# Kernel optimization log

Measured on AMD Instinct MI355X. Metric: run time of the kernel, lower is better.

The kernel has to match this reference:

```python
import jax, jax.numpy as jnp
import numpy as np

HID = 256
BATCH = 16384
L_K = 4


def _mixture(lst, Ws):
    # lst: [B, 4, H] candidate tensors; Ws: [H] scoring vector (Linear(H,1,bias=False))
    scores = jnp.einsum('bkh,h->bk', lst, Ws)            # [B, 4]
    w = jax.nn.softmax(scores, axis=-1)                  # softmax over the l=4 candidates
    out = jnp.einsum('bk,bkh->bh', w, lst)               # [B, H] mixture
    s = scores.sum(axis=0)                               # [4] summed over batch
    idx = jnp.argmax(s).astype(jnp.int32)                # routing decision
    ss = jnp.sort(s)
    margin = ss[-1] - ss[-2]                             # top-2 margin
    return out, idx, margin


def setup_inputs() -> dict:
    key = jax.random.key(0)
    ks = jax.random.split(key, 6)
    bound = 1.0 / np.sqrt(HID)
    x = jax.random.normal(ks[0], (BATCH, 1, HID), dtype=jnp.float32)
    h = jax.random.normal(ks[1], (BATCH, 1, HID), dtype=jnp.float32)
    L = jax.random.uniform(ks[2], (L_K, HID, HID), dtype=jnp.float32, minval=-bound, maxval=bound)
    R = jax.random.uniform(ks[3], (L_K, HID, HID), dtype=jnp.float32, minval=-bound, maxval=bound)
    # k=3 slots are initialized to identity / zero bias in the torch module
    L = L.at[3].set(jnp.eye(HID, dtype=jnp.float32))
    R = R.at[3].set(jnp.eye(HID, dtype=jnp.float32))
    b = jnp.zeros((L_K, HID), dtype=jnp.float32)
    Ws = jax.random.normal(ks[4], (HID,), dtype=jnp.float32) * bound
    return {'x': x, 'h': h, 'L': L, 'R': R, 'b': b, 'Ws': Ws}


def reference(x, h, L, R, b, Ws):
    x2 = x[:, 0, :]  # [B, H]
    h2 = h[:, 0, :]  # [B, H]

    z1 = jax.nn.sigmoid(x2 @ L[0] + h2 @ R[0] + b[0])
    r = jax.nn.sigmoid(x2 @ L[1] + h2 @ R[1] + b[1])
    z2 = jax.nn.sigmoid(x2 @ L[0] + h2 @ R[0] + b[0])  # identical expression in the source

    def lin(A, Bv):
        # candidate set: A @ L[k] + Bv @ R[k] + b[k] for k in 0..3 -> [B, 4, H]
        return jnp.einsum('bh,khd->bkd', A, L) + jnp.einsum('bh,khd->bkd', Bv, R) + b[None]

    rh, i1, m1 = _mixture(lin(h2, r), Ws)
    h_tilde, i2, m2 = _mixture(lin(x2, rh), Ws)

    omz_cand = 1.0 - (jnp.einsum('bh,khd->bkd', z1, R) + b[None])
    oneMinusZ1, i3, m3 = _mixture(omz_cand, Ws)

    zh_cand = jnp.einsum('bh,khd->bkd', h_tilde, L) * jnp.einsum('bh,khd->bkd', oneMinusZ1, R) + b[None]
    zh_tilde, i4, m4 = _mixture(zh_cand, Ws)

    z2h_cand = jnp.einsum('bh,khd->bkd', h2, L) * jnp.einsum('bh,khd->bkd', z2, R) + b[None]
    z2h, i5, m5 = _mixture(z2h_cand, Ws)

    h_next, i6, m6 = _mixture(lin(zh_tilde, z2h), Ws)

    G_structure = jnp.concatenate([
        jnp.array([0, 1, 0], dtype=jnp.int32),
        jnp.stack([i1, i2, i3, i4, i5, i6]),
    ])
    G_node = jnp.stack([z1, r, z2, rh, h_tilde, oneMinusZ1, zh_tilde, z2h, h_next], axis=1)  # [B, 9, H]
    margins = jnp.stack([m1, m2, m3, m4, m5, m6])
    return h_next[:, None, :], G_structure, G_node, margins
```

## Files before the change

### kernel.cpp

```cpp
#include <hip/hip_runtime.h>

typedef __bf16 bf16_t;
typedef bf16_t bf16x8 __attribute__((ext_vector_type(8)));
typedef float f32x4 __attribute__((ext_vector_type(4)));

#define BATCH 16384
#define HID 256

__device__ __forceinline__ ushort f2b(float f) {
  union { float f; unsigned u; } v; v.f = f;
  unsigned u = v.u;
  unsigned r = (u + 0x7fffu + ((u >> 16) & 1u)) >> 16;
  return (ushort)r;
}
__device__ __forceinline__ float b2f(ushort u) {
  union { unsigned u; float f; } v; v.u = ((unsigned)u) << 16; return v.f;
}
__device__ __forceinline__ void loadbf4(const ushort* __restrict__ p, float* o) {
  uint2 q = *(const uint2*)p;
  o[0] = b2f((ushort)(q.x & 0xffffu));
  o[1] = b2f((ushort)(q.x >> 16));
  o[2] = b2f((ushort)(q.y & 0xffffu));
  o[3] = b2f((ushort)(q.y >> 16));
}
__device__ __forceinline__ uint2 packbf4(const float* v) {
  uint2 q;
  q.x = (unsigned)f2b(v[0]) | ((unsigned)f2b(v[1]) << 16);
  q.y = (unsigned)f2b(v[2]) | ((unsigned)f2b(v[3]) << 16);
  return q;
}

__global__ __launch_bounds__(256)
void f2b2_kernel(const float* __restrict__ a, const float* __restrict__ b,
                 ushort* __restrict__ oa, ushort* __restrict__ ob) {
  int bid = blockIdx.x;
  const float* in = (bid < 4096) ? a : b;
  ushort* out     = (bid < 4096) ? oa : ob;
  int t = (bid & 4095) * 256 + threadIdx.x;
  float4 v = *(const float4*)(in + (size_t)t * 4);
  float q[4] = {v.x, v.y, v.z, v.w};
  *(uint2*)(out + (size_t)t * 4) = packbf4(q);
}

__global__ __launch_bounds__(256)
void wt2_kernel(const float* __restrict__ L, const float* __restrict__ R,
                ushort* __restrict__ Lt, ushort* __restrict__ Rt) {
  int bid = blockIdx.x;
  const float* W = (bid < 1024) ? L : R;
  ushort* Wt     = (bid < 1024) ? Lt : Rt;
  int idx = (bid & 1023) * 256 + threadIdx.x;
  int c = idx >> 8, hh = idx & 255;
  int ks = c >> 8, d = c & 255;
  Wt[idx] = f2b(W[ks * 65536 + hh * 256 + d]);
}

struct GJob {
  const ushort* A; const ushort* B; ushort* out;
  int nx;
  int nblocks;
};

__global__ __launch_bounds__(256, 4)
void gemm3_kernel(GJob j0, GJob j1, GJob j2, int o1, int o2) {
  __shared__ __align__(16) ushort SH[16384];

  const int bid = blockIdx.x;
  GJob j; int lbid;
  if (bid < o1)      { j = j0; lbid = bid; }
  else if (bid < o2) { j = j1; lbid = bid - o1; }
  else               { j = j2; lbid = bid - o2; }

  const int tid  = threadIdx.x;
  const int lane = tid & 63;
  const int wave = tid >> 6;

  const int qq  = j.nblocks >> 3;
  const int id2 = (lbid & 7) * qq + (lbid >> 3);
  int cn, cm;
  if (j.nx == 8) { cn = id2 & 7; cm = id2 >> 3; }
  else           { cn = id2 & 3; cm = id2 >> 2; }
  const int bm = cm * 128;
  const int bn = cn * 128;

  const int wm   = (wave >> 1) * 64;
  const int wn   = (wave & 1) * 64;
  const int row  = lane & 15;
  const int quad = lane >> 4;
  const int gq   = (quad ^ ((row >> 1) & 3)) << 3;

  const int l4   = lane >> 2;
  const int gsrc = (lane & 3) ^ ((lane >> 3) & 3);

  f32x4 acc[4][4] = {};

  auto stage = [&](int buf, int kt) {
    const int k0 = kt * 32;
    for (int i = 0; i < 2; ++i) {
      const int ci = wave * 2 + i;
      const int r  = ci * 16 + l4;
      __builtin_amdgcn_global_load_lds(
          (const __attribute__((address_space(1))) void*)(j.A + (size_t)(bm + r) * 256 + k0 + gsrc * 8),
          (__attribute__((address_space(3))) void*)&SH[buf * 4096 + ci * 512], 16, 0, 0);
      __builtin_amdgcn_global_load_lds(
          (const __attribute__((address_space(1))) void*)(j.B + (size_t)(bn + r) * 256 + k0 + gsrc * 8),
          (__attribute__((address_space(3))) void*)&SH[8192 + buf * 4096 + ci * 512], 16, 0, 0);
    }
  };

  auto compute = [&](int buf) {
    bf16x8 af[4], bf[4];
    for (int f = 0; f < 4; ++f) {
      const int ar = wm + f * 16 + row;
      af[f] = *(const bf16x8*)&SH[buf * 4096 + ar * 32 + gq];
      const int br = wn + f * 16 + row;
      bf[f] = *(const bf16x8*)&SH[8192 + buf * 4096 + br * 32 + gq];
    }
    __builtin_amdgcn_s_setprio(1);
    for (int ti = 0; ti < 4; ++ti)
      for (int tj = 0; tj < 4; ++tj)
        acc[ti][tj] = __builtin_amdgcn_mfma_f32_16x16x32_bf16(af[ti], bf[tj], acc[ti][tj], 0, 0, 0);
    __builtin_amdgcn_s_setprio(0);
  };

  stage(0, 0);
  __syncthreads();
#pragma unroll
  for (int t = 0; t < 8; ++t) {
    if (t < 7) stage((t + 1) & 1, t + 1);
    __builtin_amdgcn_sched_barrier(0);
    compute(t & 1);
    if (t < 7) __syncthreads();
  }

  __syncthreads();
  const int N = j.nx * 128;
  ushort* cw = &SH[wave * 4096];
  for (int ti = 0; ti < 4; ++ti)
    for (int tj = 0; tj < 4; ++tj)
      for (int r2 = 0; r2 < 4; ++r2) {
        const int r = ti * 16 + quad * 4 + r2;
        const int c = tj * 16 + row;
        cw[r * 64 + ((((c >> 3) ^ (r & 7)) << 3) | (c & 7))] = f2b(acc[ti][tj][r2]);
      }
  for (int it = 0; it < 8; ++it) {
    const int lr = it * 8 + (lane >> 3);
    const int ch = lane & 7;
    const int gp = ch ^ (lr & 7);
    uint4 v = *(const uint4*)&cw[lr * 64 + gp * 8];
    *(uint4*)(j.out + (size_t)(bm + wm + lr) * N + bn + wn + ch * 8) = v;
  }
}

__global__ __launch_bounds__(256)
void sig_kernel(const ushort* __restrict__ P0, const ushort* __restrict__ P2,
                const float* __restrict__ bias, float* __restrict__ gnode,
                ushort* __restrict__ z1b, ushort* __restrict__ rb) {
  int t = blockIdx.x * 256 + threadIdx.x;
  int b = t >> 6;
  int d0 = (t & 63) * 4;
  float xl[4], hr[4], z[4], r[4];
  loadbf4(P0 + (size_t)b * 1024 + d0, xl);
  loadbf4(P2 + (size_t)b * 512 + d0, hr);
  float4 bb = *(const float4*)(bias + d0);
  float bbb[4] = {bb.x, bb.y, bb.z, bb.w};
  for (int i = 0; i < 4; ++i) z[i] = 1.0f / (1.0f + expf(-(xl[i] + hr[i] + bbb[i])));
  size_t g = (size_t)b * 2304 + d0;
  float4 zv = {z[0], z[1], z[2], z[3]};
  *(float4*)(gnode + g) = zv;
  *(float4*)(gnode + g + 512) = zv;
  *(uint2*)(z1b + (size_t)b * 256 + d0) = packbf4(z);
  loadbf4(P0 + (size_t)b * 1024 + 256 + d0, xl);
  loadbf4(P2 + (size_t)b * 512 + 256 + d0, hr);
  float4 b1 = *(const float4*)(bias + 256 + d0);
  float b1b[4] = {b1.x, b1.y, b1.z, b1.w};
  for (int i = 0; i < 4; ++i) r[i] = 1.0f / (1.0f + expf(-(xl[i] + hr[i] + b1b[i])));
  float4 rv = {r[0], r[1], r[2], r[3]};
  *(float4*)(gnode + g + 256) = rv;
  *(uint2*)(rb + (size_t)b * 256 + d0) = packbf4(r);
}

struct MixJob {
  const ushort* P1; const ushort* P2;
  float* gnode; ushort* act; float* hnext; float* part;
  int mode;
};

__global__ __launch_bounds__(256)
void mixN_kernel(MixJob j0, MixJob j1, MixJob j2, const float* __restrict__ bias,
                 const float* __restrict__ Ws) {
  const int jb = blockIdx.x >> 12;
  const MixJob j = (jb == 0) ? j0 : (jb == 1) ? j1 : j2;
  const int lb = blockIdx.x & 4095;

  const int tid  = threadIdx.x;
  const int wave = tid >> 6;
  const int lane = tid & 63;
  const int row  = lb * 4 + wave;
  const int d0   = lane * 4;
  float c[4][4];
  float sp[4];
  float4 w4 = *(const float4*)(Ws + d0);
  float ws4[4] = {w4.x, w4.y, w4.z, w4.w};
  for (int k = 0; k < 4; ++k) {
    float p1[4];
    loadbf4(j.P1 + (size_t)row * 1024 + k * 256 + d0, p1);
    float4 bb = *(const float4*)(bias + k * 256 + d0);
    float bv[4] = {bb.x, bb.y, bb.z, bb.w};
    float v[4];
    if (j.mode == 0) {
      float p2[4];
      loadbf4(j.P2 + (size_t)row * 1024 + k * 256 + d0, p2);
      for (int i = 0; i < 4; ++i) v[i] = p1[i] + p2[i] + bv[i];
    } else if (j.mode == 1) {
      for (int i = 0; i < 4; ++i) v[i] = 1.0f - (p1[i] + bv[i]);
    } else {
      float p2[4];
      loadbf4(j.P2 + (size_t)row * 1024 + k * 256 + d0, p2);
      for (int i = 0; i < 4; ++i) v[i] = p1[i] * p2[i] + bv[i];
    }
    float s = 0.f;
    for (int i = 0; i < 4; ++i) { c[k][i] = v[i]; s += v[i] * ws4[i]; }
    sp[k] = s;
  }
  for (int m = 1; m < 64; m <<= 1)
    for (int k = 0; k < 4; ++k) sp[k] += __shfl_xor(sp[k], m, 64);
  float mx = fmaxf(fmaxf(sp[0], sp[1]), fmaxf(sp[2], sp[3]));
  float e0 = expf(sp[0] - mx), e1 = expf(sp[1] - mx), e2 = expf(sp[2] - mx), e3 = expf(sp[3] - mx);
  float inv = 1.0f / (e0 + e1 + e2 + e3);
  float w0 = e0 * inv, w1 = e1 * inv, w2 = e2 * inv, w3 = e3 * inv;
  float o[4];
  for (int i = 0; i < 4; ++i) o[i] = w0 * c[0][i] + w1 * c[1][i] + w2 * c[2][i] + w3 * c[3][i];
  size_t g = (size_t)row * 2304 + d0;
  float4 ov = {o[0], o[1], o[2], o[3]};
  *(float4*)(j.gnode + g) = ov;
  if (j.act) *(uint2*)(j.act + (size_t)row * 256 + d0) = packbf4(o);
  if (j.hnext) *(float4*)(j.hnext + (size_t)row * 256 + d0) = ov;
  __shared__ float sred[4][4];
  if (lane == 0) for (int k = 0; k < 4; ++k) sred[wave][k] = sp[k];
  __syncthreads();
  if (tid < 4)
    j.part[lb * 4 + tid] = sred[0][tid] + sred[1][tid] + sred[2][tid] + sred[3][tid];
}

__global__ __launch_bounds__(256)
void fin_kernel(const float* __restrict__ part, float* __restrict__ gs,
                float* __restrict__ margins) {
  __shared__ float red[256][4];
  __shared__ float sfin[6][4];
  int tid = threadIdx.x;
  for (int si = 0; si < 6; ++si) {
    float a[4] = {0.f, 0.f, 0.f, 0.f};
    for (int i = 0; i < 16; ++i) {
      const float* p = part + ((size_t)si * 4096 + tid + 256 * i) * 4;
      for (int k = 0; k < 4; ++k) a[k] += p[k];
    }
    for (int k = 0; k < 4; ++k) red[tid][k] = a[k];
    __syncthreads();
    for (int st = 128; st >= 1; st >>= 1) {
      if (tid < st) for (int k = 0; k < 4; ++k) red[tid][k] += red[tid + st][k];
      __syncthreads();
    }
    if (tid == 0) for (int k = 0; k < 4; ++k) sfin[si][k] = red[0][k];
    __syncthreads();
  }
  if (tid == 0) {
    gs[0] = 0.f; gs[1] = 1.f; gs[2] = 0.f;
    for (int si = 0; si < 6; ++si) {
      float s[4] = {sfin[si][0], sfin[si][1], sfin[si][2], sfin[si][3]};
      int idx = 0; float best = s[0];
      for (int k = 1; k < 4; ++k) if (s[k] > best) { best = s[k]; idx = k; }
      float second = -3.4e38f;
      for (int k = 0; k < 4; ++k) if (k != idx) second = fmaxf(second, s[k]);
      gs[3 + si] = (float)idx;
      margins[si] = best - second;
    }
  }
}

extern "C" void kernel_launch(void* const* d_in, const int* in_sizes, int n_in,
                              void* d_out, int out_size, void* d_ws, size_t ws_size,
                              hipStream_t stream) {
  const float* x    = (const float*)d_in[0];
  const float* h    = (const float*)d_in[1];
  const float* L    = (const float*)d_in[2];
  const float* R    = (const float*)d_in[3];
  const float* bias = (const float*)d_in[4];
  const float* Ws   = (const float*)d_in[5];

  float* out        = (float*)d_out;
  float* out_hnext  = out;
  float* out_gs     = out + 4194304;
  float* out_gnode  = out + 4194313;
  float* out_marg   = out + 41943049;

  ushort* P0   = (ushort*)d_ws;
  ushort* P1   = P0 + (size_t)BATCH * 1024;
  ushort* P2   = P1 + (size_t)BATCH * 1024;
  ushort* P3   = P2 + (size_t)BATCH * 1024;
  ushort* x2b  = P3 + (size_t)BATCH * 1024;
  ushort* h2b  = x2b + (size_t)BATCH * HID;
  ushort* z1b  = h2b + (size_t)BATCH * HID;
  ushort* rb   = z1b + (size_t)BATCH * HID;
  ushort* rhb  = rb  + (size_t)BATCH * HID;
  ushort* htb  = rhb + (size_t)BATCH * HID;
  ushort* omzb = htb + (size_t)BATCH * HID;
  ushort* ztb  = omzb + (size_t)BATCH * HID;
  ushort* z2hb = ztb + (size_t)BATCH * HID;
  ushort* Lt   = z2hb + (size_t)BATCH * HID;
  ushort* Rt   = Lt + 1024 * 256;
  float*  part = (float*)(Rt + 1024 * 256);

  f2b2_kernel<<<8192, 256, 0, stream>>>(x, h, x2b, h2b);
  wt2_kernel<<<2048, 256, 0, stream>>>(L, R, Lt, Rt);

  GJob jz = {};

  {
    GJob a = {x2b, Lt, P0, 8, 1024};
    GJob b = {h2b, Lt, P1, 8, 1024};
    GJob c = {h2b, Rt, P2, 4, 512};
    gemm3_kernel<<<2560, 256, 0, stream>>>(a, b, c, 1024, 2048);
  }
  sig_kernel<<<4096, 256, 0, stream>>>(P0, P2, bias, out_gnode, z1b, rb);
  {
    GJob a = {rb,  Rt, P2, 8, 1024};
    GJob b = {z1b, Rt, P3, 8, 1024};
    gemm3_kernel<<<2048, 256, 0, stream>>>(a, b, jz, 1024, 2048);
  }
  {
    MixJob m0 = {P1, P2, out_gnode + 3 * 256, rhb,  nullptr, part + 0 * 16384, 0};
    MixJob m1 = {P3, P3, out_gnode + 5 * 256, omzb, nullptr, part + 2 * 16384, 1};
    MixJob m2 = {P1, P3, out_gnode + 7 * 256, z2hb, nullptr, part + 4 * 16384, 2};
    mixN_kernel<<<12288, 256, 0, stream>>>(m0, m1, m2, bias, Ws);
  }
  {
    GJob a = {rhb,  Rt, P2, 8, 1024};
    GJob b = {omzb, Rt, P3, 8, 1024};
    GJob c = {z2hb, Rt, P1, 8, 1024};
    gemm3_kernel<<<3072, 256, 0, stream>>>(a, b, c, 1024, 2048);
  }
  {
    MixJob m0 = {P0, P2, out_gnode + 4 * 256, htb, nullptr, part + 1 * 16384, 0};
    mixN_kernel<<<4096, 256, 0, stream>>>(m0, m0, m0, bias, Ws);
  }
  {
    GJob a = {htb, Lt, P0, 8, 1024};
    gemm3_kernel<<<1024, 256, 0, stream>>>(a, jz, jz, 1024, 1024);
  }
  {
    MixJob m0 = {P0, P3, out_gnode + 6 * 256, ztb, nullptr, part + 3 * 16384, 2};
    mixN_kernel<<<4096, 256, 0, stream>>>(m0, m0, m0, bias, Ws);
  }
  {
    GJob a = {ztb, Lt, P2, 8, 1024};
    gemm3_kernel<<<1024, 256, 0, stream>>>(a, jz, jz, 1024, 1024);
  }
  {
    MixJob m0 = {P2, P1, out_gnode + 8 * 256, nullptr, out_hnext, part + 5 * 16384, 0};
    mixN_kernel<<<4096, 256, 0, stream>>>(m0, m0, m0, bias, Ws);
  }
  fin_kernel<<<1, 256, 0, stream>>>(part, out_gs, out_marg);
}
```

Baseline: 449.4 us.

## Fuse additive L/R candidate GEMMs via concatenated K dimension with bias epilogue

The additive candidate sets (A@L[k] + B@R[k] + b[k]) are now computed as one GEMM with K=512 by streaming A·L and then B·R into the same accumulator, and the bias is added in the GEMM epilogue. Separate P buffers and the add in the mixture kernel go away, and a new mixture mode reads the finished candidates directly. The first GEMM also narrows its x@L job to only the two slices that are needed. This cuts intermediate bf16 writes and reads and the number of GEMM outputs, in exchange for longer K loops and more buffer aliasing that has to stay correct.

Result: no change. 455.5 us (+1.4%).

```diff
diff --git a/kernel.cpp b/kernel.cpp
--- a/kernel.cpp
+++ b/kernel.cpp
@@ -6,6 +6,8 @@
 
 #define BATCH 16384
 #define HID 256
+
+template<int N> struct IC { static constexpr int v = N; };
 
 __device__ __forceinline__ ushort f2b(float f) {
   union { float f; unsigned u; } v; v.f = f;
@@ -55,13 +57,18 @@
 }
 
 struct GJob {
-  const ushort* A; const ushort* B; ushort* out;
+  const ushort* A; const ushort* A2;
+  const ushort* B; const ushort* B2;
+  ushort* out;
   int nx;
+  int nk;
   int nblocks;
+  int epi;
 };
 
 __global__ __launch_bounds__(256, 4)
-void gemm3_kernel(GJob j0, GJob j1, GJob j2, int o1, int o2) {
+void gemm3_kernel(GJob j0, GJob j1, GJob j2, int o1, int o2,
+                  const float* __restrict__ bias) {
   __shared__ __align__(16) ushort SH[16384];
 
   const int bid = blockIdx.x;
@@ -94,15 +101,17 @@
   f32x4 acc[4][4] = {};
 
   auto stage = [&](int buf, int kt) {
-    const int k0 = kt * 32;
+    const ushort* Ab = (kt < 8) ? j.A : j.A2;
+    const ushort* Bb = (kt < 8) ? j.B : j.B2;
+    const int k0 = (kt & 7) * 32;
     for (int i = 0; i < 2; ++i) {
       const int ci = wave * 2 + i;
       const int r  = ci * 16 + l4;
       __builtin_amdgcn_global_load_lds(
-          (const __attribute__((address_space(1))) void*)(j.A + (size_t)(bm + r) * 256 + k0 + gsrc * 8),
+          (const __attribute__((address_space(1))) void*)(Ab + (size_t)(bm + r) * 256 + k0 + gsrc * 8),
           (__attribute__((address_space(3))) void*)&SH[buf * 4096 + ci * 512], 16, 0, 0);
       __builtin_amdgcn_global_load_lds(
-          (const __attribute__((address_space(1))) void*)(j.B + (size_t)(bn + r) * 256 + k0 + gsrc * 8),
+          (const __attribute__((address_space(1))) void*)(Bb + (size_t)(bn + r) * 256 + k0 + gsrc * 8),
           (__attribute__((address_space(3))) void*)&SH[8192 + buf * 4096 + ci * 512], 16, 0, 0);
     }
   };
@@ -122,25 +131,32 @@
     __builtin_amdgcn_s_setprio(0);
   };
 
-  stage(0, 0);
-  __syncthreads();
+  auto pipe = [&](auto NTC) {
+    constexpr int NT = decltype(NTC)::v;
+    stage(0, 0);
+    __syncthreads();
 #pragma unroll
-  for (int t = 0; t < 8; ++t) {
-    if (t < 7) stage((t + 1) & 1, t + 1);
-    __builtin_amdgcn_sched_barrier(0);
-    compute(t & 1);
-    if (t < 7) __syncthreads();
-  }
+    for (int t = 0; t < NT; ++t) {
+      if (t < NT - 1) stage((t + 1) & 1, t + 1);
+      __builtin_amdgcn_sched_barrier(0);
+      compute(t & 1);
+      if (t < NT - 1) __syncthreads();
+    }
+  };
+  if (j.nk == 16) pipe(IC<16>{}); else pipe(IC<8>{});
 
   __syncthreads();
   const int N = j.nx * 128;
+  float b4[4] = {0.f, 0.f, 0.f, 0.f};
+  if (j.epi == 1)
+    for (int tj = 0; tj < 4; ++tj) b4[tj] = bias[bn + wn + tj * 16 + row];
   ushort* cw = &SH[wave * 4096];
   for (int ti = 0; ti < 4; ++ti)
     for (int tj = 0; tj < 4; ++tj)
       for (int r2 = 0; r2 < 4; ++r2) {
         const int r = ti * 16 + quad * 4 + r2;
         const int c = tj * 16 + row;
-        cw[r * 64 + ((((c >> 3) ^ (r & 7)) << 3) | (c & 7))] = f2b(acc[ti][tj][r2]);
+        cw[r * 64 + ((((c >> 3) ^ (r & 7)) << 3) | (c & 7))] = f2b(acc[ti][tj][r2] + b4[tj]);
       }
   for (int it = 0; it < 8; ++it) {
     const int lr = it * 8 + (lane >> 3);
@@ -159,7 +175,7 @@
   int b = t >> 6;
   int d0 = (t & 63) * 4;
   float xl[4], hr[4], z[4], r[4];
-  loadbf4(P0 + (size_t)b * 1024 + d0, xl);
+  loadbf4(P0 + (size_t)b * 512 + d0, xl);
   loadbf4(P2 + (size_t)b * 512 + d0, hr);
   float4 bb = *(const float4*)(bias + d0);
   float bbb[4] = {bb.x, bb.y, bb.z, bb.w};
@@ -169,7 +185,7 @@
   *(float4*)(gnode + g) = zv;
   *(float4*)(gnode + g + 512) = zv;
   *(uint2*)(z1b + (size_t)b * 256 + d0) = packbf4(z);
-  loadbf4(P0 + (size_t)b * 1024 + 256 + d0, xl);
+  loadbf4(P0 + (size_t)b * 512 + 256 + d0, xl);
   loadbf4(P2 + (size_t)b * 512 + 256 + d0, hr);
   float4 b1 = *(const float4*)(bias + 256 + d0);
   float b1b[4] = {b1.x, b1.y, b1.z, b1.w};
@@ -204,19 +220,23 @@
   for (int k = 0; k < 4; ++k) {
     float p1[4];
     loadbf4(j.P1 + (size_t)row * 1024 + k * 256 + d0, p1);
-    float4 bb = *(const float4*)(bias + k * 256 + d0);
-    float bv[4] = {bb.x, bb.y, bb.z, bb.w};
     float v[4];
-    if (j.mode == 0) {
-      float p2[4];
-      loadbf4(j.P2 + (size_t)row * 1024 + k * 256 + d0, p2);
-      for (int i = 0; i < 4; ++i) v[i] = p1[i] + p2[i] + bv[i];
-    } else if (j.mode == 1) {
-      for (int i = 0; i < 4; ++i) v[i] = 1.0f - (p1[i] + bv[i]);
+    if (j.mode == 3) {
+      for (int i = 0; i < 4; ++i) v[i] = p1[i];
     } else {
-      float p2[4];
-      loadbf4(j.P2 + (size_t)row * 1024 + k * 256 + d0, p2);
-      for (int i = 0; i < 4; ++i) v[i] = p1[i] * p2[i] + bv[i];
+      float4 bb = *(const float4*)(bias + k * 256 + d0);
+      float bv[4] = {bb.x, bb.y, bb.z, bb.w};
+      if (j.mode == 1) {
+        for (int i = 0; i < 4; ++i) v[i] = 1.0f - (p1[i] + bv[i]);
+      } else if (j.mode == 0) {
+        float p2[4];
+        loadbf4(j.P2 + (size_t)row * 1024 + k * 256 + d0, p2);
+        for (int i = 0; i < 4; ++i) v[i] = p1[i] + p2[i] + bv[i];
+      } else {
+        float p2[4];
+        loadbf4(j.P2 + (size_t)row * 1024 + k * 256 + d0, p2);
+        for (int i = 0; i < 4; ++i) v[i] = p1[i] * p2[i] + bv[i];
+      }
     }
     float s = 0.f;
     for (int i = 0; i < 4; ++i) { c[k][i] = v[i]; s += v[i] * ws4[i]; }
@@ -316,47 +336,46 @@
   GJob jz = {};
 
   {
-    GJob a = {x2b, Lt, P0, 8, 1024};
-    GJob b = {h2b, Lt, P1, 8, 1024};
-    GJob c = {h2b, Rt, P2, 4, 512};
-    gemm3_kernel<<<2560, 256, 0, stream>>>(a, b, c, 1024, 2048);
+    GJob a = {x2b, nullptr, Lt, nullptr, P0, 4, 8, 512, 0};
+    GJob b = {h2b, nullptr, Lt, nullptr, P1, 8, 8, 1024, 0};
+    GJob c = {h2b, nullptr, Rt, nullptr, P2, 4, 8, 512, 0};
+    gemm3_kernel<<<2048, 256, 0, stream>>>(a, b, c, 512, 1536, bias);
   }
   sig_kernel<<<4096, 256, 0, stream>>>(P0, P2, bias, out_gnode, z1b, rb);
   {
-    GJob a = {rb,  Rt, P2, 8, 1024};
-    GJob b = {z1b, Rt, P3, 8, 1024};
-    gemm3_kernel<<<2048, 256, 0, stream>>>(a, b, jz, 1024, 2048);
-  }
-  {
-    MixJob m0 = {P1, P2, out_gnode + 3 * 256, rhb,  nullptr, part + 0 * 16384, 0};
-    MixJob m1 = {P3, P3, out_gnode + 5 * 256, omzb, nullptr, part + 2 * 16384, 1};
-    MixJob m2 = {P1, P3, out_gnode + 7 * 256, z2hb, nullptr, part + 4 * 16384, 2};
+    GJob a = {h2b, rb, Lt, Rt, P2, 8, 16, 1024, 1};
+    GJob b = {z1b, nullptr, Rt, nullptr, P3, 8, 8, 1024, 0};
+    gemm3_kernel<<<2048, 256, 0, stream>>>(a, b, jz, 1024, 2048, bias);
+  }
+  {
+    MixJob m0 = {P2, nullptr, out_gnode + 3 * 256, rhb,  nullptr, part + 0 * 16384, 3};
+    MixJob m1 = {P3, nullptr, out_gnode + 5 * 256, omzb, nullptr, part + 2 * 16384, 1};
+    MixJob m2 = {P1, P3,      out_gnode + 7 * 256, z2hb, nullptr, part + 4 * 16384, 2};
     mixN_kernel<<<12288, 256, 0, stream>>>(m0, m1, m2, bias, Ws);
   }
   {
-    GJob a = {rhb,  Rt, P2, 8, 1024};
-    GJob b = {omzb, Rt, P3, 8, 1024};
-    GJob c = {z2hb, Rt, P1, 8, 1024};
-    gemm3_kernel<<<3072, 256, 0, stream>>>(a, b, c, 1024, 2048);
-  }
-  {
-    MixJob m0 = {P0, P2, out_gnode + 4 * 256, htb, nullptr, part + 1 * 16384, 0};
+    GJob a = {x2b, rhb, Lt, Rt, P0, 8, 16, 1024, 1};
+    GJob b = {omzb, nullptr, Rt, nullptr, P2, 8, 8, 1024, 0};
+    gemm3_kernel<<<2048, 256, 0, stream>>>(a, b, jz, 1024, 2048, bias);
+  }
+  {
+    MixJob m0 = {P0, nullptr, out_gnode + 4 * 256, htb, nullptr, part + 1 * 16384, 3};
     mixN_kernel<<<4096, 256, 0, stream>>>(m0, m0, m0, bias, Ws);
   }
   {
-    GJob a = {htb, Lt, P0, 8, 1024};
-    gemm3_kernel<<<1024, 256, 0, stream>>>(a, jz, jz, 1024, 1024);
-  }
-  {
-    MixJob m0 = {P0, P3, out_gnode + 6 * 256, ztb, nullptr, part + 3 * 16384, 2};
+    GJob a = {htb, nullptr, Lt, nullptr, P1, 8, 8, 1024, 0};
+    gemm3_kernel<<<1024, 256, 0, stream>>>(a, jz, jz, 1024, 1024, bias);
+  }
+  {
+    MixJob m0 = {P1, P2, out_gnode + 6 * 256, ztb, nullptr, part + 3 * 16384, 2};
     mixN_kernel<<<4096, 256, 0, stream>>>(m0, m0, m0, bias, Ws);
   }
   {
-    GJob a = {ztb, Lt, P2, 8, 1024};
-    gemm3_kernel<<<1024, 256, 0, stream>>>(a, jz, jz, 1024, 1024);
-  }
-  {
-    MixJob m0 = {P2, P1, out_gnode + 8 * 256, nullptr, out_hnext, part + 5 * 16384, 0};
+    GJob a = {ztb, z2hb, Lt, Rt, P3, 8, 16, 1024, 1};
+    gemm3_kernel<<<1024, 256, 0, stream>>>(a, jz, jz, 1024, 1024, bias);
+  }
+  {
+    MixJob m0 = {P3, nullptr, out_gnode + 8 * 256, nullptr, out_hnext, part + 5 * 16384, 3};
     mixN_kernel<<<4096, 256, 0, stream>>>(m0, m0, m0, bias, Ws);
   }
   fin_kernel<<<1, 256, 0, stream>>>(part, out_gs, out_marg);
```
